# Kernel tuning notes

Hardware: AMD Instinct MI355X
Metric: run time of the kernel (lower is better)

The kernel has to match this reference:

```python
import jax, jax.numpy as jnp
import numpy as np

N = 100000
E = 1600000
IN_DIM = 128
HID = 16      # per-head dim
HEADS = 4
FEAT = HID * HEADS  # 64
OUT_DIM = 64
EPS = 0.5
LAYERS = 2


def setup_inputs() -> dict:
    key = jax.random.key(0)
    ks = jax.random.split(key, 8)
    return {
        "h": jax.random.normal(ks[0], (N, IN_DIM), dtype=jnp.float32),
        "src": jax.random.randint(ks[1], (E,), 0, N, dtype=jnp.int64),
        "dst": jax.random.randint(ks[2], (E,), 0, N, dtype=jnp.int64),
        "t1_W": jax.random.normal(ks[3], (IN_DIM, FEAT), dtype=jnp.float32) * 0.1,
        "t1_b": jnp.zeros((FEAT,), dtype=jnp.float32),
        "t2_W": jax.random.normal(ks[4], (FEAT, OUT_DIM), dtype=jnp.float32) * 0.1,
        "t2_b": jnp.zeros((OUT_DIM,), dtype=jnp.float32),
        "gate_W": jax.random.normal(ks[5], (LAYERS, 2 * HID, 1), dtype=jnp.float32) * 0.2,
        "gate_b": jnp.zeros((LAYERS, 1), dtype=jnp.float32),
    }


def reference(h, src, dst, t1_W, t1_b, t2_W, t2_b, gate_W, gate_b):
    # t1 + relu
    x = jax.nn.relu(h @ t1_W + t1_b)            # [N, FEAT]
    raw = x

    # symmetric degree norm: deg^-0.5 from in-degrees (clamped at 1)
    deg = jax.ops.segment_sum(jnp.ones((E,), x.dtype), dst, num_segments=N)
    norm = jnp.clip(deg, 1.0, None) ** -0.5     # [N]

    xh = x.reshape(N, HEADS, HID)
    edge_norm = norm[dst] * norm[src]           # [E]
    h1 = raw
    # NOTE: original forward never updates x inside the loop; each layer
    # consumes the same relu(t1(h)) and only the last layer's h0 survives.
    for l in range(LAYERS):
        hs = xh[src]                            # [E, H, D] gather src
        hd = xh[dst]                            # [E, H, D] gather dst
        hcat = jnp.concatenate([hd, hs], axis=-1)  # [E, H, 2D]
        s = jnp.tanh(hcat @ gate_W[l] + gate_b[l])[..., 0]  # [E, H]
        s = s * edge_norm[:, None]
        e_h = (hs * s[..., None]).reshape(E, FEAT)          # [E, FEAT]
        h0 = jax.ops.segment_sum(e_h, dst, num_segments=N)  # scatter-sum
        h1 = EPS * raw + h0

    return h1 @ t2_W + t2_b                      # [N, OUT_DIM]
```

## Files before the change

kernel.cpp:

```cpp
#include <hip/hip_runtime.h>
#include <hip/hip_fp16.h>
#include <math.h>

#define N_NODES 100000
#define E_EDGES 1600000
#define IN_DIM  128
#define FEAT    64
#define OUT_DIM 64
#define NBKT    391
#define CAP     6144
#define RNG     4096
#define NSCB    ((E_EDGES + RNG - 1) / RNG)
#define G1B     ((N_NODES + 255) / 256)

typedef float vfloat2 __attribute__((ext_vector_type(2)));

__global__ __launch_bounds__(256) void k_binscatter(
    const int* __restrict__ src, const int* __restrict__ dst,
    int* __restrict__ bucket_cursor, int* __restrict__ binned)
{
    __shared__ int hist[NBKT];
    __shared__ int baseS[NBKT];
    __shared__ int cursor[NBKT];
    __shared__ int gbase[NBKT];
    __shared__ int sA[512], sB[512];
    __shared__ int buf[RNG];
    __shared__ unsigned short bkt[RNG];

    const int tid  = threadIdx.x;
    const int e0   = blockIdx.x * RNG;
    const int ecnt = min(RNG, E_EDGES - e0);

    for (int i = tid; i < NBKT; i += 256) hist[i] = 0;
    __syncthreads();

    int dsave[16];
#pragma unroll
    for (int k = 0; k < 16; ++k) {
        int e = e0 + k * 256 + tid;
        int d = (e < E_EDGES) ? dst[e] : -1;
        dsave[k] = d;
        if (d >= 0) atomicAdd(&hist[d >> 8], 1);
    }
    __syncthreads();

    for (int i = tid; i < 512; i += 256) sA[i] = (i < NBKT) ? hist[i] : 0;
    __syncthreads();
    int* pa = sA; int* pb = sB;
    for (int off = 1; off < 512; off <<= 1) {
        for (int i = tid; i < 512; i += 256)
            pb[i] = pa[i] + ((i >= off) ? pa[i - off] : 0);
        __syncthreads();
        int* t = pa; pa = pb; pb = t;
    }
    for (int i = tid; i < NBKT; i += 256) {
        int ex = pa[i] - hist[i];
        baseS[i]  = ex;
        cursor[i] = ex;
    }
    __syncthreads();

#pragma unroll
    for (int k = 0; k < 16; ++k) {
        int d = dsave[k];
        if (d >= 0) {
            int e   = e0 + k * 256 + tid;
            int s   = src[e];
            int b   = d >> 8;
            int pos = atomicAdd(&cursor[b], 1);
            buf[pos] = ((d & 255) << 17) | s;
            bkt[pos] = (unsigned short)b;
        }
    }
    __syncthreads();

    for (int t = tid; t < NBKT; t += 256) {
        int cnt = hist[t];
        int g   = cnt ? atomicAdd(&bucket_cursor[t], cnt) : 0;
        gbase[t] = g - baseS[t];
    }
    __syncthreads();

    for (int i = tid; i < ecnt; i += 256) {
        int b   = bkt[i];
        int off = gbase[b] + i;
        if (off < CAP) binned[b * CAP + off] = buf[i];
    }
}

__global__ __launch_bounds__(256) void k_bucketfinal(
    const int* __restrict__ binned, const int* __restrict__ bucket_cursor,
    int* __restrict__ deg, int* __restrict__ rowptr, int* __restrict__ src_sorted)
{
    __shared__ int sA[512], sB[512];
    __shared__ int hist[256];
    __shared__ int scn[256];
    __shared__ int cur[256];
    const int b   = blockIdx.x;
    const int tid = threadIdx.x;

    for (int i = tid; i < 512; i += 256) sA[i] = (i < NBKT) ? bucket_cursor[i] : 0;
    __syncthreads();
    int* pa = sA; int* pb = sB;
    for (int off = 1; off < 512; off <<= 1) {
        for (int i = tid; i < 512; i += 256)
            pb[i] = pa[i] + ((i >= off) ? pa[i - off] : 0);
        __syncthreads();
        int* t = pa; pa = pb; pb = t;
    }
    const int cnt  = bucket_cursor[b];
    const int eb   = pa[b] - cnt;
    const int base = b * CAP;
    __syncthreads();

    hist[tid] = 0;
    __syncthreads();
    for (int i = tid; i < cnt; i += 256)
        atomicAdd(&hist[binned[base + i] >> 17], 1);
    __syncthreads();

    int v = hist[tid];
    scn[tid] = v;
    __syncthreads();
    for (int off = 1; off < 256; off <<= 1) {
        int add = (tid >= off) ? scn[tid - off] : 0;
        __syncthreads();
        scn[tid] += add;
        __syncthreads();
    }
    int ex = scn[tid] - v;
    cur[tid] = ex;
    int n = b * 256 + tid;
    if (n < N_NODES) {
        deg[n]    = v;
        rowptr[n] = eb + ex;
    }
    if (b == 0 && tid == 0) rowptr[N_NODES] = E_EDGES;
    __syncthreads();

    for (int i = tid; i < cnt; i += 256) {
        int p   = binned[base + i];
        int dl  = p >> 17;
        int pos = atomicAdd(&cur[dl], 1);
        src_sorted[eb + pos] = p & 0x1FFFF;
    }
}

__global__ __launch_bounds__(256, 3) void k_gemm1(
    const float* __restrict__ h, const float* __restrict__ W1,
    const float* __restrict__ b1, const int* __restrict__ deg,
    const float* __restrict__ gate_W,
    __half* __restrict__ xs2h, unsigned int* __restrict__ xq,
    float* __restrict__ aproj, float* __restrict__ bproj)
{
    __shared__ float Ws[IN_DIM * FEAT];
    __shared__ float hT[16 * 260];
    const int tid = threadIdx.x;
    const int r0  = blockIdx.x * 256;

    for (int i = tid; i < IN_DIM * FEAT / 4; i += 256)
        ((float4*)Ws)[i] = ((const float4*)W1)[i];

    const int rg = tid >> 2;
    const int cg = tid & 3;
    const int c0 = cg * 16;
    float acc[4][16];
#pragma unroll
    for (int i = 0; i < 4; ++i)
#pragma unroll
        for (int j = 0; j < 16; ++j) acc[i][j] = 0.f;

    const int  myrow = r0 + tid;
    const bool rok   = myrow < N_NODES;

    for (int kc = 0; kc < IN_DIM / 16; ++kc) {
        float4 f[4];
        if (rok) {
            const float4* hp = (const float4*)(h + (size_t)myrow * IN_DIM + kc * 16);
            f[0] = hp[0]; f[1] = hp[1]; f[2] = hp[2]; f[3] = hp[3];
        } else {
            f[0] = f[1] = f[2] = f[3] = make_float4(0.f, 0.f, 0.f, 0.f);
        }
        __syncthreads();
#pragma unroll
        for (int q = 0; q < 4; ++q) {
            hT[(q * 4 + 0) * 260 + tid] = f[q].x;
            hT[(q * 4 + 1) * 260 + tid] = f[q].y;
            hT[(q * 4 + 2) * 260 + tid] = f[q].z;
            hT[(q * 4 + 3) * 260 + tid] = f[q].w;
        }
        __syncthreads();
#pragma unroll
        for (int kk = 0; kk < 16; ++kk) {
            float4 a4 = *(const float4*)&hT[kk * 260 + rg * 4];
            const float* wrow = &Ws[(kc * 16 + kk) * FEAT + c0];
            float4 w0 = ((const float4*)wrow)[0];
            float4 w1 = ((const float4*)wrow)[1];
            float4 w2 = ((const float4*)wrow)[2];
            float4 w3 = ((const float4*)wrow)[3];
            const float a[4] = {a4.x, a4.y, a4.z, a4.w};
            const float w[16] = {w0.x, w0.y, w0.z, w0.w, w1.x, w1.y, w1.z, w1.w,
                                 w2.x, w2.y, w2.z, w2.w, w3.x, w3.y, w3.z, w3.w};
#pragma unroll
            for (int i = 0; i < 4; ++i)
#pragma unroll
                for (int j = 0; j < 16; ++j)
                    acc[i][j] = fmaf(a[i], w[j], acc[i][j]);
        }
    }

#pragma unroll
    for (int i = 0; i < 4; ++i) {
        int r = r0 + rg * 4 + i;
        if (r >= N_NODES) continue;
        float nr = rsqrtf(fmaxf((float)deg[r], 1.f));
        float xa = 0.f, xb = 0.f;
        alignas(16) __half hv[16];
        float vs[16];
#pragma unroll
        for (int j = 0; j < 16; ++j) {
            float v = acc[i][j] + b1[c0 + j];
            v = v > 0.f ? v : 0.f;
            xa = fmaf(v, gate_W[32 + j], xa);
            xb = fmaf(v, gate_W[48 + j], xb);
            float sv = v * nr;
            vs[j] = sv;
            hv[j] = __float2half(sv);
        }
        float4* xp = (float4*)(xs2h + (size_t)r * FEAT + c0);
        xp[0] = *(const float4*)&hv[0];
        xp[1] = *(const float4*)&hv[8];
        unsigned int u[4];
#pragma unroll
        for (int q = 0; q < 4; ++q) {
            unsigned int t = 0;
            t = __builtin_amdgcn_cvt_pk_fp8_f32(vs[q*4+0], vs[q*4+1], t, false);
            t = __builtin_amdgcn_cvt_pk_fp8_f32(vs[q*4+2], vs[q*4+3], t, true);
            u[q] = t;
        }
        ((uint4*)xq)[(size_t)r * 4 + cg] = make_uint4(u[0], u[1], u[2], u[3]);
        aproj[(size_t)r * 4 + cg] = xa;
        bproj[(size_t)r * 4 + cg] = xb;
    }
}

__global__ __launch_bounds__(256) void k_aggregate(
    const uint4* __restrict__ xq4, const __half2* __restrict__ xs2h2,
    const float* __restrict__ aproj, const float* __restrict__ bproj,
    const int* __restrict__ rowptr, const int* __restrict__ src_sorted,
    const float* __restrict__ gate_b,
    const float* __restrict__ W2, const float* __restrict__ b2,
    float* __restrict__ out)
{
    __shared__ float W2s[FEAT * OUT_DIM];
    __shared__ float vbuf[4][FEAT];

    const int tid    = threadIdx.x;
    const int lane   = tid & 63;
    const int e      = lane >> 2;
    const int l4     = lane & 3;
    const int wslot  = tid >> 6;
    const int wave   = blockIdx.x * 4 + wslot;
    const int nwaves = gridDim.x * 4;
    const float gb   = gate_b[1];
    const float C    = 2.8853900817779268f;

    for (int i = tid; i < FEAT * OUT_DIM / 4; i += 256)
        ((float4*)W2s)[i] = ((const float4*)W2)[i];
    const float myb2 = b2[lane];
    __syncthreads();

    for (int n = wave; n < N_NODES; n += nwaves) {
        const int beg = rowptr[n];
        const int end = rowptr[n + 1];
        const int cnt = end - beg;
        const float a_d = aproj[(size_t)n * 4 + l4] + gb;

        float acc[16];
#pragma unroll
        for (int k = 0; k < 16; ++k) acc[k] = 0.f;

        if (cnt > 0) {
            const int last = end - 1;
            int  j0  = beg + e;
            bool ok0 = j0 < end;
            int  s0  = src_sorted[ok0 ? j0 : last];
            uint4 x0 = xq4[(size_t)s0 * 4 + l4];
            float b0 = bproj[(size_t)s0 * 4 + l4];
            int  j1  = j0 + 16;
            bool ok1 = j1 < end;
            int  s1  = src_sorted[ok1 ? j1 : last];

            for (int j = beg; j < end; j += 16) {
                const bool more = (j + 16) < end;
                uint4 x1 = make_uint4(0u, 0u, 0u, 0u);
                float b1 = 0.f;
                int   s2 = s1;
                bool  ok2 = false;
                if (more) {
                    x1 = xq4[(size_t)s1 * 4 + l4];
                    b1 = bproj[(size_t)s1 * 4 + l4];
                    int j2 = j + 32 + e;
                    ok2 = j2 < end;
                    s2 = src_sorted[ok2 ? j2 : last];
                }
                float ex = __builtin_amdgcn_exp2f(C * (a_d + b0));
                float t  = 1.f - 2.f * __builtin_amdgcn_rcpf(ex + 1.f);
                t = ok0 ? t : 0.f;
#pragma unroll
                for (int w = 0; w < 4; ++w) {
                    const unsigned int xw = ((const unsigned int*)&x0)[w];
                    vfloat2 lo = __builtin_amdgcn_cvt_pk_f32_fp8(xw, false);
                    vfloat2 hi = __builtin_amdgcn_cvt_pk_f32_fp8(xw, true);
                    acc[w * 4 + 0] = fmaf(t, lo[0], acc[w * 4 + 0]);
                    acc[w * 4 + 1] = fmaf(t, lo[1], acc[w * 4 + 1]);
                    acc[w * 4 + 2] = fmaf(t, hi[0], acc[w * 4 + 2]);
                    acc[w * 4 + 3] = fmaf(t, hi[1], acc[w * 4 + 3]);
                }
                if (more) {
                    x0 = x1; b0 = b1; ok0 = ok1; ok1 = ok2; s1 = s2;
                }
            }
        }

        const bool elo = (e & 1) == 0;
        float r8[8];
#pragma unroll
        for (int i = 0; i < 8; ++i) {
            float give = elo ? acc[8 + i] : acc[i];
            float got  = __shfl_xor(give, 4, 64);
            r8[i] = (elo ? acc[i] : acc[8 + i]) + got;
        }
        const bool e2lo = (e & 2) == 0;
        float v4[4];
#pragma unroll
        for (int i = 0; i < 4; ++i) {
            float give = e2lo ? r8[4 + i] : r8[i];
            float got  = __shfl_xor(give, 8, 64);
            v4[i] = (e2lo ? r8[i] : r8[4 + i]) + got;
        }
#pragma unroll
        for (int i = 0; i < 4; ++i) v4[i] += __shfl_xor(v4[i], 16, 64);
#pragma unroll
        for (int i = 0; i < 4; ++i) v4[i] += __shfl_xor(v4[i], 32, 64);

        const float dg = fmaxf((float)cnt, 1.f);
        const float nd = rsqrtf(dg);
        const float sd = dg * nd;

        if (e < 4) {
            const int q = ((e & 1) << 1) | ((e >> 1) & 1);
            const int Q = l4 * 4 + q;
            const __half2* hp = xs2h2 + (size_t)n * 32 + Q * 2;
            float2 fa = __half22float2(hp[0]);
            float2 fb = __half22float2(hp[1]);
            float4 v;
            v.x = fmaf(0.5f * sd, fa.x, v4[0] * nd);
            v.y = fmaf(0.5f * sd, fa.y, v4[1] * nd);
            v.z = fmaf(0.5f * sd, fb.x, v4[2] * nd);
            v.w = fmaf(0.5f * sd, fb.y, v4[3] * nd);
            *(float4*)&vbuf[wslot][Q * 4] = v;
        }
        float oacc = myb2;
        const float* vb = vbuf[wslot];
#pragma unroll
        for (int fq = 0; fq < 16; ++fq) {
            float4 vv = *(const float4*)&vb[fq * 4];
            oacc = fmaf(vv.x, W2s[(fq * 4 + 0) * OUT_DIM + lane], oacc);
            oacc = fmaf(vv.y, W2s[(fq * 4 + 1) * OUT_DIM + lane], oacc);
            oacc = fmaf(vv.z, W2s[(fq * 4 + 2) * OUT_DIM + lane], oacc);
            oacc = fmaf(vv.w, W2s[(fq * 4 + 3) * OUT_DIM + lane], oacc);
        }
        out[(size_t)n * OUT_DIM + lane] = oacc;
    }
}

extern "C" void kernel_launch(void* const* d_in, const int* in_sizes, int n_in,
                              void* d_out, int out_size, void* d_ws, size_t ws_size,
                              hipStream_t stream)
{
    const float* h   = (const float*)d_in[0];
    const int*   src = (const int*)d_in[1];
    const int*   dst = (const int*)d_in[2];
    const float* W1  = (const float*)d_in[3];
    const float* b1  = (const float*)d_in[4];
    const float* W2  = (const float*)d_in[5];
    const float* b2  = (const float*)d_in[6];
    const float* gW  = (const float*)d_in[7];
    const float* gb  = (const float*)d_in[8];
    float* out = (float*)d_out;

    int* bucket_cursor = (int*)d_ws;
    int* binned        = bucket_cursor + NBKT;
    int* src_sorted    = binned + (size_t)NBKT * CAP;
    int* rowptr        = src_sorted + E_EDGES;
    int* deg           = rowptr + (N_NODES + 1);
    float* aproj       = (float*)(deg + N_NODES);
    float* bproj       = aproj + (size_t)N_NODES * 4;
    __half* xs2h       = (__half*)(bproj + (size_t)N_NODES * 4);
    unsigned int* xq   = (unsigned int*)(xs2h + (size_t)N_NODES * FEAT);

    hipMemsetAsync(bucket_cursor, 0, NBKT * sizeof(int), stream);

    k_binscatter <<<NSCB, 256, 0, stream>>>(src, dst, bucket_cursor, binned);
    k_bucketfinal<<<NBKT, 256, 0, stream>>>(binned, bucket_cursor, deg, rowptr, src_sorted);
    k_gemm1      <<<G1B, 256, 0, stream>>>(h, W1, b1, deg, gW, xs2h, xq, aproj, bproj);
    k_aggregate  <<<2048, 256, 0, stream>>>((const uint4*)xq, (const __half2*)xs2h,
                                            aproj, bproj, rowptr, src_sorted, gb,
                                            W2, b2, out);
}
```

Measured before the change: 247.5 us.

## Replace bucketed CSR build with global-atomic counting sort; shuffle-based output GEMV

The two-pass shared-memory bucket sort that built the CSR by destination is replaced with a plain counting sort. It now runs a global atomic histogram of dst, a two-kernel block scan into rowptr and cursor, and an atomic scatter of src into src_sorted. This removes the large binned staging buffer and its CAP overflow limit, at the cost of millions of contended global atomics. Separately, the aggregate kernel's final W2 projection now broadcasts per-lane values with cross-lane shuffles instead of staging through shared memory. That drops the LDS write/read round trip but adds 64 shuffles per node.

After: 435.5 us. 1.76x slower.

```diff
diff --git a/kernel.cpp b/kernel.cpp
--- a/kernel.cpp
+++ b/kernel.cpp
@@ -8,43 +8,47 @@
 #define FEAT    64
 #define OUT_DIM 64
 #define NBKT    391
-#define CAP     6144
-#define RNG     4096
-#define NSCB    ((E_EDGES + RNG - 1) / RNG)
 #define G1B     ((N_NODES + 255) / 256)
 
 typedef float vfloat2 __attribute__((ext_vector_type(2)));
 
-__global__ __launch_bounds__(256) void k_binscatter(
-    const int* __restrict__ src, const int* __restrict__ dst,
-    int* __restrict__ bucket_cursor, int* __restrict__ binned)
-{
-    __shared__ int hist[NBKT];
-    __shared__ int baseS[NBKT];
-    __shared__ int cursor[NBKT];
-    __shared__ int gbase[NBKT];
+__global__ __launch_bounds__(256) void k_hist(
+    const int* __restrict__ dst, int* __restrict__ deg)
+{
+    const int i4 = blockIdx.x * 256 + threadIdx.x;
+    if (i4 < E_EDGES / 4) {
+        int4 d = ((const int4*)dst)[i4];
+        atomicAdd(&deg[d.x], 1);
+        atomicAdd(&deg[d.y], 1);
+        atomicAdd(&deg[d.z], 1);
+        atomicAdd(&deg[d.w], 1);
+    }
+}
+
+__global__ __launch_bounds__(256) void k_scanA(
+    const int* __restrict__ deg, int* __restrict__ bsum)
+{
+    __shared__ int wsum[4];
+    const int tid = threadIdx.x;
+    const int n   = blockIdx.x * 256 + tid;
+    int v = (n < N_NODES) ? deg[n] : 0;
+#pragma unroll
+    for (int off = 1; off < 64; off <<= 1) v += __shfl_xor(v, off, 64);
+    if ((tid & 63) == 0) wsum[tid >> 6] = v;
+    __syncthreads();
+    if (tid == 0) bsum[blockIdx.x] = wsum[0] + wsum[1] + wsum[2] + wsum[3];
+}
+
+__global__ __launch_bounds__(256) void k_scanB(
+    const int* __restrict__ deg, const int* __restrict__ bsum,
+    int* __restrict__ rowptr, int* __restrict__ cursor)
+{
     __shared__ int sA[512], sB[512];
-    __shared__ int buf[RNG];
-    __shared__ unsigned short bkt[RNG];
-
-    const int tid  = threadIdx.x;
-    const int e0   = blockIdx.x * RNG;
-    const int ecnt = min(RNG, E_EDGES - e0);
-
-    for (int i = tid; i < NBKT; i += 256) hist[i] = 0;
-    __syncthreads();
-
-    int dsave[16];
-#pragma unroll
-    for (int k = 0; k < 16; ++k) {
-        int e = e0 + k * 256 + tid;
-        int d = (e < E_EDGES) ? dst[e] : -1;
-        dsave[k] = d;
-        if (d >= 0) atomicAdd(&hist[d >> 8], 1);
-    }
-    __syncthreads();
-
-    for (int i = tid; i < 512; i += 256) sA[i] = (i < NBKT) ? hist[i] : 0;
+    __shared__ int scn[256];
+    const int b   = blockIdx.x;
+    const int tid = threadIdx.x;
+
+    for (int i = tid; i < 512; i += 256) sA[i] = (i < NBKT) ? bsum[i] : 0;
     __syncthreads();
     int* pa = sA; int* pb = sB;
     for (int off = 1; off < 512; off <<= 1) {
@@ -53,73 +57,11 @@
         __syncthreads();
         int* t = pa; pa = pb; pb = t;
     }
-    for (int i = tid; i < NBKT; i += 256) {
-        int ex = pa[i] - hist[i];
-        baseS[i]  = ex;
-        cursor[i] = ex;
-    }
-    __syncthreads();
-
-#pragma unroll
-    for (int k = 0; k < 16; ++k) {
-        int d = dsave[k];
-        if (d >= 0) {
-            int e   = e0 + k * 256 + tid;
-            int s   = src[e];
-            int b   = d >> 8;
-            int pos = atomicAdd(&cursor[b], 1);
-            buf[pos] = ((d & 255) << 17) | s;
-            bkt[pos] = (unsigned short)b;
-        }
-    }
-    __syncthreads();
-
-    for (int t = tid; t < NBKT; t += 256) {
-        int cnt = hist[t];
-        int g   = cnt ? atomicAdd(&bucket_cursor[t], cnt) : 0;
-        gbase[t] = g - baseS[t];
-    }
-    __syncthreads();
-
-    for (int i = tid; i < ecnt; i += 256) {
-        int b   = bkt[i];
-        int off = gbase[b] + i;
-        if (off < CAP) binned[b * CAP + off] = buf[i];
-    }
-}
-
-__global__ __launch_bounds__(256) void k_bucketfinal(
-    const int* __restrict__ binned, const int* __restrict__ bucket_cursor,
-    int* __restrict__ deg, int* __restrict__ rowptr, int* __restrict__ src_sorted)
-{
-    __shared__ int sA[512], sB[512];
-    __shared__ int hist[256];
-    __shared__ int scn[256];
-    __shared__ int cur[256];
-    const int b   = blockIdx.x;
-    const int tid = threadIdx.x;
-
-    for (int i = tid; i < 512; i += 256) sA[i] = (i < NBKT) ? bucket_cursor[i] : 0;
-    __syncthreads();
-    int* pa = sA; int* pb = sB;
-    for (int off = 1; off < 512; off <<= 1) {
-        for (int i = tid; i < 512; i += 256)
-            pb[i] = pa[i] + ((i >= off) ? pa[i - off] : 0);
-        __syncthreads();
-        int* t = pa; pa = pb; pb = t;
-    }
-    const int cnt  = bucket_cursor[b];
-    const int eb   = pa[b] - cnt;
-    const int base = b * CAP;
-    __syncthreads();
-
-    hist[tid] = 0;
-    __syncthreads();
-    for (int i = tid; i < cnt; i += 256)
-        atomicAdd(&hist[binned[base + i] >> 17], 1);
-    __syncthreads();
-
-    int v = hist[tid];
+    const int base = pa[b] - bsum[b];
+    __syncthreads();
+
+    const int n = b * 256 + tid;
+    int v = (n < N_NODES) ? deg[n] : 0;
     scn[tid] = v;
     __syncthreads();
     for (int off = 1; off < 256; off <<= 1) {
@@ -128,21 +70,26 @@
         scn[tid] += add;
         __syncthreads();
     }
-    int ex = scn[tid] - v;
-    cur[tid] = ex;
-    int n = b * 256 + tid;
+    const int ex = base + scn[tid] - v;
     if (n < N_NODES) {
-        deg[n]    = v;
-        rowptr[n] = eb + ex;
+        rowptr[n] = ex;
+        cursor[n] = ex;
     }
     if (b == 0 && tid == 0) rowptr[N_NODES] = E_EDGES;
-    __syncthreads();
-
-    for (int i = tid; i < cnt; i += 256) {
-        int p   = binned[base + i];
-        int dl  = p >> 17;
-        int pos = atomicAdd(&cur[dl], 1);
-        src_sorted[eb + pos] = p & 0x1FFFF;
+}
+
+__global__ __launch_bounds__(256) void k_scatter(
+    const int* __restrict__ src, const int* __restrict__ dst,
+    int* __restrict__ cursor, int* __restrict__ src_sorted)
+{
+    const int i4 = blockIdx.x * 256 + threadIdx.x;
+    if (i4 < E_EDGES / 4) {
+        int4 s = ((const int4*)src)[i4];
+        int4 d = ((const int4*)dst)[i4];
+        int p0 = atomicAdd(&cursor[d.x], 1); src_sorted[p0] = s.x;
+        int p1 = atomicAdd(&cursor[d.y], 1); src_sorted[p1] = s.y;
+        int p2 = atomicAdd(&cursor[d.z], 1); src_sorted[p2] = s.z;
+        int p3 = atomicAdd(&cursor[d.w], 1); src_sorted[p3] = s.w;
     }
 }
 
@@ -253,21 +200,20 @@
     float* __restrict__ out)
 {
     __shared__ float W2s[FEAT * OUT_DIM];
-    __shared__ float vbuf[4][FEAT];
 
     const int tid    = threadIdx.x;
     const int lane   = tid & 63;
     const int e      = lane >> 2;
     const int l4     = lane & 3;
-    const int wslot  = tid >> 6;
-    const int wave   = blockIdx.x * 4 + wslot;
+    const int wave   = blockIdx.x * 4 + (tid >> 6);
     const int nwaves = gridDim.x * 4;
     const float gb   = gate_b[1];
     const float C    = 2.8853900817779268f;
 
     for (int i = tid; i < FEAT * OUT_DIM / 4; i += 256)
         ((float4*)W2s)[i] = ((const float4*)W2)[i];
-    const float myb2 = b2[lane];
+    const float  myb2 = b2[lane];
+    const float* w2l  = W2s + lane;
     __syncthreads();
 
     for (int n = wave; n < N_NODES; n += nwaves) {
@@ -348,28 +294,31 @@
         const float nd = rsqrtf(dg);
         const float sd = dg * nd;
 
-        if (e < 4) {
+        {
             const int q = ((e & 1) << 1) | ((e >> 1) & 1);
             const int Q = l4 * 4 + q;
             const __half2* hp = xs2h2 + (size_t)n * 32 + Q * 2;
             float2 fa = __half22float2(hp[0]);
             float2 fb = __half22float2(hp[1]);
-            float4 v;
-            v.x = fmaf(0.5f * sd, fa.x, v4[0] * nd);
-            v.y = fmaf(0.5f * sd, fa.y, v4[1] * nd);
-            v.z = fmaf(0.5f * sd, fb.x, v4[2] * nd);
-            v.w = fmaf(0.5f * sd, fb.y, v4[3] * nd);
-            *(float4*)&vbuf[wslot][Q * 4] = v;
-        }
+            v4[0] = fmaf(0.5f * sd, fa.x, v4[0] * nd);
+            v4[1] = fmaf(0.5f * sd, fa.y, v4[1] * nd);
+            v4[2] = fmaf(0.5f * sd, fb.x, v4[2] * nd);
+            v4[3] = fmaf(0.5f * sd, fb.y, v4[3] * nd);
+        }
+
         float oacc = myb2;
-        const float* vb = vbuf[wslot];
-#pragma unroll
-        for (int fq = 0; fq < 16; ++fq) {
-            float4 vv = *(const float4*)&vb[fq * 4];
-            oacc = fmaf(vv.x, W2s[(fq * 4 + 0) * OUT_DIM + lane], oacc);
-            oacc = fmaf(vv.y, W2s[(fq * 4 + 1) * OUT_DIM + lane], oacc);
-            oacc = fmaf(vv.z, W2s[(fq * 4 + 2) * OUT_DIM + lane], oacc);
-            oacc = fmaf(vv.w, W2s[(fq * 4 + 3) * OUT_DIM + lane], oacc);
+#pragma unroll
+        for (int hq = 0; hq < 4; ++hq) {
+#pragma unroll
+            for (int qq = 0; qq < 4; ++qq) {
+                const int sl = ((((qq >> 1) & 1) | ((qq & 1) << 1)) << 2) + hq;
+                const int f0 = hq * 16 + qq * 4;
+#pragma unroll
+                for (int i = 0; i < 4; ++i) {
+                    float bc = __shfl(v4[i], sl, 64);
+                    oacc = fmaf(bc, w2l[(f0 + i) * OUT_DIM], oacc);
+                }
+            }
         }
         out[(size_t)n * OUT_DIM + lane] = oacc;
     }
@@ -390,22 +339,25 @@
     const float* gb  = (const float*)d_in[8];
     float* out = (float*)d_out;
 
-    int* bucket_cursor = (int*)d_ws;
-    int* binned        = bucket_cursor + NBKT;
-    int* src_sorted    = binned + (size_t)NBKT * CAP;
-    int* rowptr        = src_sorted + E_EDGES;
-    int* deg           = rowptr + (N_NODES + 1);
-    float* aproj       = (float*)(deg + N_NODES);
-    float* bproj       = aproj + (size_t)N_NODES * 4;
-    __half* xs2h       = (__half*)(bproj + (size_t)N_NODES * 4);
-    unsigned int* xq   = (unsigned int*)(xs2h + (size_t)N_NODES * FEAT);
-
-    hipMemsetAsync(bucket_cursor, 0, NBKT * sizeof(int), stream);
-
-    k_binscatter <<<NSCB, 256, 0, stream>>>(src, dst, bucket_cursor, binned);
-    k_bucketfinal<<<NBKT, 256, 0, stream>>>(binned, bucket_cursor, deg, rowptr, src_sorted);
-    k_gemm1      <<<G1B, 256, 0, stream>>>(h, W1, b1, deg, gW, xs2h, xq, aproj, bproj);
-    k_aggregate  <<<2048, 256, 0, stream>>>((const uint4*)xq, (const __half2*)xs2h,
-                                            aproj, bproj, rowptr, src_sorted, gb,
-                                            W2, b2, out);
-}
+    int* deg        = (int*)d_ws;
+    int* cursor     = deg + N_NODES;
+    int* bsum       = cursor + N_NODES;
+    int* rowptr     = bsum + NBKT;
+    int* src_sorted = rowptr + (N_NODES + 1);
+    float* aproj    = (float*)(src_sorted + E_EDGES);
+    float* bproj    = aproj + (size_t)N_NODES * 4;
+    __half* xs2h    = (__half*)(bproj + (size_t)N_NODES * 4);
+    unsigned int* xq = (unsigned int*)(xs2h + (size_t)N_NODES * FEAT);
+
+    hipMemsetAsync(deg, 0, N_NODES * sizeof(int), stream);
+
+    const int hblk = (E_EDGES / 4 + 255) / 256;
+    k_hist   <<<hblk, 256, 0, stream>>>(dst, deg);
+    k_scanA  <<<NBKT, 256, 0, stream>>>(deg, bsum);
+    k_scanB  <<<NBKT, 256, 0, stream>>>(deg, bsum, rowptr, cursor);
+    k_scatter<<<hblk, 256, 0, stream>>>(src, dst, cursor, src_sorted);
+    k_gemm1  <<<G1B, 256, 0, stream>>>(h, W1, b1, deg, gW, xs2h, xq, aproj, bproj);
+    k_aggregate<<<2048, 256, 0, stream>>>((const uint4*)xq, (const __half2*)xs2h,
+                                          aproj, bproj, rowptr, src_sorted, gb,
+                                          W2, b2, out);
+}
```
